# Performance work log

Hardware: AMD Instinct MI355X
Metric: run time of the kernel (lower is better)

## Reference

```python
import jax, jax.numpy as jnp
import numpy as np

B, S, D = 1, 2048, 4096
N_Q, N_KV, HD = 32, 8, 128
N_REP = N_Q // N_KV
WINDOW = 1024
NEG = -1e9


def setup_inputs() -> dict:
    key = jax.random.key(0)
    ks = jax.random.split(key, 6)
    x = jax.random.normal(ks[0], (B, S, D), dtype=jnp.float32)
    # RoPE frequencies (Llama-style): theta = 10000^{-2i/HD}
    inv_freq = 1.0 / (10000.0 ** (np.arange(0, HD, 2, dtype=np.float32) / HD))
    t = np.arange(S, dtype=np.float32)
    ang = np.outer(t, inv_freq)  # [S, HD//2]
    freqs_cos = jnp.asarray(np.cos(ang), dtype=jnp.float32)
    freqs_sin = jnp.asarray(np.sin(ang), dtype=jnp.float32)
    # additive causal mask [S, S]: 0 on/below diag, -1e9 above
    mask = jnp.where(jnp.tril(jnp.ones((S, S), dtype=bool)), 0.0, NEG).astype(jnp.float32)
    scale = 0.02
    w_q = jax.random.normal(ks[1], (D, N_Q * HD), dtype=jnp.float32) * scale
    w_k = jax.random.normal(ks[2], (D, N_KV * HD), dtype=jnp.float32) * scale
    w_v = jax.random.normal(ks[3], (D, N_KV * HD), dtype=jnp.float32) * scale
    w_o = jax.random.normal(ks[4], (N_Q * HD, D), dtype=jnp.float32) * scale
    return {"x": x, "freqs_cos": freqs_cos, "freqs_sin": freqs_sin, "mask": mask,
            "w_q": w_q, "w_k": w_k, "w_v": w_v, "w_o": w_o}


def _rope(t, cos, sin):
    # t: [B, S, H, HD]; cos/sin: [S, HD//2] -> complex multiply on pairs
    tp = t.reshape(*t.shape[:-1], HD // 2, 2)
    e, o = tp[..., 0], tp[..., 1]
    c = cos[None, :, None, :]
    s = sin[None, :, None, :]
    re = e * c - o * s
    ro = e * s + o * c
    return jnp.stack([re, ro], axis=-1).reshape(t.shape)


def reference(x, freqs_cos, freqs_sin, mask, w_q, w_k, w_v, w_o):
    b, s, _ = x.shape
    xq = (x @ w_q).reshape(b, s, N_Q, HD)
    xk = (x @ w_k).reshape(b, s, N_KV, HD)
    xv = (x @ w_v).reshape(b, s, N_KV, HD)
    xq = _rope(xq, freqs_cos, freqs_sin)
    xk = _rope(xk, freqs_cos, freqs_sin)
    # GQA head repeat
    keys = jnp.repeat(xk, N_REP, axis=2)    # [b, s, N_Q, HD]
    values = jnp.repeat(xv, N_REP, axis=2)
    q = xq.transpose(0, 2, 1, 3)            # [b, h, s, hd]
    k = keys.transpose(0, 2, 1, 3)
    v = values.transpose(0, 2, 1, 3)
    scores = jnp.einsum('bhqd,bhkd->bhqk', q, k) / jnp.sqrt(jnp.float32(HD))
    scores = scores + mask[None, None, :, :]
    # sliding-window band: attend only to keys within WINDOW positions back
    idx = jnp.arange(s)
    diff = idx[:, None] - idx[None, :]
    sliding = (diff >= 0) & (diff < WINDOW)
    scores = jnp.where(sliding[None, None, :, :], scores, NEG)
    probs = jax.nn.softmax(scores, axis=-1).astype(q.dtype)
    out = jnp.einsum('bhqk,bhkd->bhqd', probs, v)
    out = out.transpose(0, 2, 1, 3).reshape(b, s, N_Q * HD)
    return out @ w_o
```

## Files before the change

kernel.cpp:

```cpp
#include <hip/hip_runtime.h>

typedef unsigned short u16;
typedef unsigned int u32;
typedef __bf16 bf16x8 __attribute__((ext_vector_type(8)));
typedef __bf16 bf16x4 __attribute__((ext_vector_type(4)));
typedef float f32x4 __attribute__((ext_vector_type(4)));

#define MFMA16(a, b, c) __builtin_amdgcn_mfma_f32_16x16x32_bf16(a, b, c, 0, 0, 0)

__device__ __forceinline__ u16 f2bf(float f) {
  u32 u = __float_as_uint(f);
  u += 0x7FFFu + ((u >> 16) & 1u);
  return (u16)(u >> 16);
}
__device__ __forceinline__ float bf2f(u16 h) {
  return __uint_as_float(((u32)h) << 16);
}

__device__ __forceinline__ void gload_lds16(const u16* g, u16* l) {
  __builtin_amdgcn_global_load_lds((__attribute__((address_space(1))) void*)g,
                                   (__attribute__((address_space(3))) void*)l,
                                   16, 0, 0);
}

__global__ __launch_bounds__(256) void cvt_x(const float* __restrict__ in,
                                             u16* __restrict__ out) {
  int i = (blockIdx.x * 256 + threadIdx.x) * 4;
  float4 v = *(const float4*)&in[i];
  ushort4 o;
  o.x = f2bf(v.x);
  o.y = f2bf(v.y);
  o.z = f2bf(v.z);
  o.w = f2bf(v.w);
  *(ushort4*)&out[i] = o;
}

__global__ __launch_bounds__(256) void tbf_f2b(const float* __restrict__ in,
                                               u16* __restrict__ out,
                                               int ldin, int ldout) {
  __shared__ float tile[64][65];
  const int t = threadIdx.x;
  const int c4 = t & 15;
  const int rb = t >> 4;
  const int r0 = blockIdx.y * 64;
  const int c0 = blockIdx.x * 64;
#pragma unroll
  for (int p = 0; p < 4; p++) {
    int r = p * 16 + rb;
    float4 v = *(const float4*)&in[(size_t)(r0 + r) * ldin + c0 + c4 * 4];
    tile[r][c4 * 4 + 0] = v.x;
    tile[r][c4 * 4 + 1] = v.y;
    tile[r][c4 * 4 + 2] = v.z;
    tile[r][c4 * 4 + 3] = v.w;
  }
  __syncthreads();
#pragma unroll
  for (int p = 0; p < 4; p++) {
    int oc = p * 16 + rb;
    ushort4 v;
    v.x = f2bf(tile[c4 * 4 + 0][oc]);
    v.y = f2bf(tile[c4 * 4 + 1][oc]);
    v.z = f2bf(tile[c4 * 4 + 2][oc]);
    v.w = f2bf(tile[c4 * 4 + 3][oc]);
    *(ushort4*)&out[(size_t)(c0 + oc) * ldout + r0 + c4 * 4] = v;
  }
}

__global__ __launch_bounds__(256) void tbf_b(const u16* __restrict__ in,
                                             u16* __restrict__ out,
                                             int ldin, int ldout) {
  __shared__ u16 tile[64][68];
  const int t = threadIdx.x;
  const int c4 = t & 15;
  const int rb = t >> 4;
  const int r0 = blockIdx.y * 64;
  const int c0 = blockIdx.x * 64;
#pragma unroll
  for (int p = 0; p < 4; p++) {
    int r = p * 16 + rb;
    ushort4 v = *(const ushort4*)&in[(size_t)(r0 + r) * ldin + c0 + c4 * 4];
    *(ushort4*)&tile[r][c4 * 4] = v;
  }
  __syncthreads();
#pragma unroll
  for (int p = 0; p < 4; p++) {
    int oc = p * 16 + rb;
    ushort4 v;
    v.x = tile[c4 * 4 + 0][oc];
    v.y = tile[c4 * 4 + 1][oc];
    v.z = tile[c4 * 4 + 2][oc];
    v.w = tile[c4 * 4 + 3][oc];
    *(ushort4*)&out[(size_t)(c0 + oc) * ldout + r0 + c4 * 4] = v;
  }
}

template <int BM, int BN, int WM, int WN, int F32OUT>
__global__ __launch_bounds__(512, 2) void gemm3(const u16* __restrict__ A,
                                                const u16* __restrict__ B,
                                                void* __restrict__ Cv,
                                                int K, int ldc) {
  constexpr int R = BM / WM / 16;
  constexpr int C = BN / WN / 16;
  constexpr int LA = (BM * 4) / 512;
  constexpr int EXTRA = BN * 4 - 512;
  constexpr int MG = (2048 / BM) / 8;
  __shared__ __attribute__((aligned(16))) u16 As[3][BM * 32];
  __shared__ __attribute__((aligned(16))) u16 Bs[3][BN * 32];
  const int tid = threadIdx.x;
  const int wave = tid >> 6;
  const int lane = tid & 63;
  const int l16 = lane & 15;
  const int quad = lane >> 4;
  const int wm = wave / WN;
  const int wn = wave % WN;
  const int id = blockIdx.x;
  const int bm = ((id & 7) * MG + ((id >> 3) % MG)) * BM;
  const int bn0 = ((id >> 3) / MG) * BN;

  const u16* srcA[LA];
#pragma unroll
  for (int m = 0; m < LA; m++) {
    int c = m * 512 + tid;
    int r = c >> 2;
    int hl = (c & 3) ^ (r & 3) ^ ((r >> 2) & 3);
    srcA[m] = A + (size_t)(bm + r) * K + hl * 8;
  }
  const u16* srcB0;
  const u16* srcB1;
  {
    int c = tid, r = c >> 2;
    int hl = (c & 3) ^ (r & 3) ^ ((r >> 2) & 3);
    srcB0 = B + (size_t)(bn0 + r) * K + hl * 8;
    c = 512 + tid;
    r = c >> 2;
    int r2 = r < BN ? r : 0;
    hl = (c & 3) ^ (r2 & 3) ^ ((r2 >> 2) & 3);
    srcB1 = B + (size_t)(bn0 + r2) * K + hl * 8;
  }

  f32x4 acc[R][C];
#pragma unroll
  for (int i = 0; i < R; i++)
#pragma unroll
    for (int j = 0; j < C; j++) acc[i][j] = (f32x4){0.f, 0.f, 0.f, 0.f};

  auto stage = [&](int kt, int nb2) {
    const int ko = kt * 32;
#pragma unroll
    for (int m = 0; m < LA; m++)
      gload_lds16(srcA[m] + ko, &As[nb2][(m * 512 + tid) * 8]);
    gload_lds16(srcB0 + ko, &Bs[nb2][tid * 8]);
    if constexpr (EXTRA == 512) {
      gload_lds16(srcB1 + ko, &Bs[nb2][(512 + tid) * 8]);
    } else if constexpr (EXTRA > 0) {
      if (tid < EXTRA) gload_lds16(srcB1 + ko, &Bs[nb2][(512 + tid) * 8]);
    }
  };

  const int NT = K >> 5;
  stage(0, 0);
  stage(1, 1);
  int nb = 0, ns = 2;
  for (int t = 0; t < NT; ++t) {
    if (t == NT - 1) {
      asm volatile("s_waitcnt vmcnt(0)" ::: "memory");
    } else if constexpr (EXTRA == 512) {
      asm volatile("s_waitcnt vmcnt(3)" ::: "memory");
    } else {
      if (wave < 4)
        asm volatile("s_waitcnt vmcnt(4)" ::: "memory");
      else
        asm volatile("s_waitcnt vmcnt(3)" ::: "memory");
    }
    __builtin_amdgcn_sched_barrier(0);
    __builtin_amdgcn_s_barrier();
    __builtin_amdgcn_sched_barrier(0);
    if (t + 2 < NT) stage(t + 2, ns);

    const u16* as = &As[nb][0];
    const u16* bs = &Bs[nb][0];
    bf16x8 bfr[C];
#pragma unroll
    for (int j = 0; j < C; j++) {
      int r = wn * (C * 16) + j * 16 + l16;
      bfr[j] = *(const bf16x8*)&bs[r * 32 +
                                   ((quad ^ (r & 3) ^ ((r >> 2) & 3)) << 3)];
    }
    bf16x8 afr[R];
#pragma unroll
    for (int i = 0; i < R; i++) {
      int r = wm * (R * 16) + i * 16 + l16;
      afr[i] = *(const bf16x8*)&as[r * 32 +
                                   ((quad ^ (r & 3) ^ ((r >> 2) & 3)) << 3)];
    }
    __builtin_amdgcn_s_setprio(1);
#pragma unroll
    for (int i = 0; i < R; i++)
#pragma unroll
      for (int j = 0; j < C; j++)
        acc[i][j] = MFMA16(afr[i], bfr[j], acc[i][j]);
    __builtin_amdgcn_s_setprio(0);
    __builtin_amdgcn_sched_barrier(0);
    nb = (nb == 2) ? 0 : nb + 1;
    ns = (ns == 2) ? 0 : ns + 1;
  }

  const int crow0 = bm + wm * (R * 16);
  const int ccol0 = bn0 + wn * (C * 16);
  if constexpr (F32OUT) {
    float* Cp = (float*)Cv;
#pragma unroll
    for (int i = 0; i < R; i++)
#pragma unroll
      for (int j = 0; j < C; j++)
#pragma unroll
        for (int rr = 0; rr < 4; rr++) {
          int row = crow0 + i * 16 + quad * 4 + rr;
          int col = ccol0 + j * 16 + l16;
          Cp[(size_t)row * ldc + col] = acc[i][j][rr];
        }
  } else {
    u16* Cp = (u16*)Cv;
#pragma unroll
    for (int i = 0; i < R; i++)
#pragma unroll
      for (int j = 0; j < C; j++)
#pragma unroll
        for (int rr = 0; rr < 4; rr++) {
          int row = crow0 + i * 16 + quad * 4 + rr;
          int col = ccol0 + j * 16 + l16;
          Cp[(size_t)row * ldc + col] = f2bf(acc[i][j][rr]);
        }
  }
}

__global__ __launch_bounds__(256) void rope_k(u16* __restrict__ qkv,
                                              const float* __restrict__ fc,
                                              const float* __restrict__ fs) {
  int idx = blockIdx.x * 256 + threadIdx.x;
  int j = idx & 63;
  int rem = idx >> 6;
  int head = rem % 40;
  int s = rem / 40;
  float c = fc[s * 64 + j];
  float sn = fs[s * 64 + j];
  int col = (head < 32) ? (head * 128 + 2 * j) : (4096 + (head - 32) * 128 + 2 * j);
  u32* p = (u32*)&qkv[(size_t)s * 6144 + col];
  u32 v = *p;
  float e = bf2f((u16)(v & 0xFFFFu));
  float o = bf2f((u16)(v >> 16));
  float re = e * c - o * sn;
  float ro = e * sn + o * c;
  *p = (u32)f2bf(re) | ((u32)f2bf(ro) << 16);
}

__global__ __launch_bounds__(256) void attn_k(const u16* __restrict__ qkv,
                                              const u16* __restrict__ vt,
                                              u16* __restrict__ outb) {
  __shared__ __attribute__((aligned(16))) u16 Kb[2][32 * 128];
  __shared__ __attribute__((aligned(16))) u16 Vb[2][128 * 32];
  __shared__ __attribute__((aligned(16))) u16 plds[4][32 * 36];
  const int h = blockIdx.x;
  const int q0 = blockIdx.y * 128;
  const int t = threadIdx.x;
  const int wave = t >> 6;
  const int lane = t & 63;
  const int l16 = lane & 15;
  const int quad = lane >> 4;
  const int hkv = h >> 2;
  const int qw = q0 + wave * 32;
  u16* myp = &plds[wave][0];

  bf16x8 qa[2][4];
#pragma unroll
  for (int i = 0; i < 2; i++)
#pragma unroll
    for (int kc = 0; kc < 4; kc++)
      qa[i][kc] = *(const bf16x8*)&qkv[(size_t)(qw + i * 16 + l16) * 6144 +
                                       h * 128 + kc * 32 + quad * 8];

  f32x4 o[2][8];
#pragma unroll
  for (int i = 0; i < 2; i++)
#pragma unroll
    for (int d = 0; d < 8; d++) o[i][d] = (f32x4){0.f, 0.f, 0.f, 0.f};
  float lloc[2][4] = {{0.f, 0.f, 0.f, 0.f}, {0.f, 0.f, 0.f, 0.f}};

  const int kb_start = (q0 - 1023 > 0 ? q0 - 1023 : 0) & ~31;
  const int kb_last = q0 + 96;
  const float sc = 0.08838834764831845f;

  const int kr0 = t >> 4, kc0s = t & 15;
  const int kr1 = (256 + t) >> 4, kc1s = t & 15;
  const int vr0 = t >> 2, vc0s = t & 3;
  const int vr1 = (256 + t) >> 2, vc1s = t & 3;
  const u16* kg = qkv + 4096 + hkv * 128;
  const u16* vg = vt + (size_t)hkv * 128 * 2048;

#define STAGE(kb_, nb_)                                                        \
  do {                                                                         \
    int kb__ = (kb_);                                                          \
    gload_lds16(&kg[(size_t)(kb__ + kr0) * 6144 + (kc0s ^ (kr0 & 15)) * 8],    \
                &Kb[nb_][t * 8]);                                              \
    gload_lds16(&kg[(size_t)(kb__ + kr1) * 6144 + (kc1s ^ (kr1 & 15)) * 8],    \
                &Kb[nb_][2048 + t * 8]);                                       \
    gload_lds16(&vg[(size_t)vr0 * 2048 + kb__ + (vc0s ^ (vr0 & 3)) * 8],       \
                &Vb[nb_][t * 8]);                                              \
    gload_lds16(&vg[(size_t)vr1 * 2048 + kb__ + (vc1s ^ (vr1 & 3)) * 8],       \
                &Vb[nb_][2048 + t * 8]);                                       \
  } while (0)

  STAGE(kb_start, 0);
  int cur = 0;

  for (int kb = kb_start; kb <= kb_last; kb += 32) {
    __syncthreads();
    if (kb + 32 <= kb_last) STAGE(kb + 32, cur ^ 1);
    const u16* kcur = &Kb[cur][0];
    const u16* vcur = &Vb[cur][0];

    f32x4 s0[2] = {(f32x4){0.f, 0.f, 0.f, 0.f}, (f32x4){0.f, 0.f, 0.f, 0.f}};
    f32x4 s1[2] = {(f32x4){0.f, 0.f, 0.f, 0.f}, (f32x4){0.f, 0.f, 0.f, 0.f}};
#pragma unroll
    for (int kc = 0; kc < 4; kc++) {
      int ch = ((kc * 4 + quad) ^ l16) * 8;
      bf16x8 b0 = *(const bf16x8*)&kcur[l16 * 128 + ch];
      bf16x8 b1 = *(const bf16x8*)&kcur[(l16 + 16) * 128 + ch];
      s0[0] = MFMA16(qa[0][kc], b0, s0[0]);
      s1[0] = MFMA16(qa[0][kc], b1, s1[0]);
      s0[1] = MFMA16(qa[1][kc], b0, s0[1]);
      s1[1] = MFMA16(qa[1][kc], b1, s1[1]);
    }

    float p0[2][4], p1[2][4];
    bool fast = (kb + 31 <= qw) && (qw + 31 - kb <= 1023);
    if (fast) {
#pragma unroll
      for (int i = 0; i < 2; i++)
#pragma unroll
        for (int r = 0; r < 4; r++) {
          p0[i][r] = __expf(s0[i][r] * sc);
          p1[i][r] = __expf(s1[i][r] * sc);
        }
    } else {
#pragma unroll
      for (int i = 0; i < 2; i++)
#pragma unroll
        for (int r = 0; r < 4; r++) {
          int row = qw + i * 16 + quad * 4 + r;
          int col0 = kb + l16;
          int col1 = col0 + 16;
          bool v0 = (col0 <= row) && (row - col0 < 1024);
          bool v1 = (col1 <= row) && (row - col1 < 1024);
          p0[i][r] = v0 ? __expf(s0[i][r] * sc) : 0.f;
          p1[i][r] = v1 ? __expf(s1[i][r] * sc) : 0.f;
        }
    }
#pragma unroll
    for (int i = 0; i < 2; i++)
#pragma unroll
      for (int r = 0; r < 4; r++) {
        lloc[i][r] += p0[i][r] + p1[i][r];
        myp[(i * 16 + quad * 4 + r) * 36 + l16] = f2bf(p0[i][r]);
        myp[(i * 16 + quad * 4 + r) * 36 + l16 + 16] = f2bf(p1[i][r]);
      }
    asm volatile("s_waitcnt lgkmcnt(0)" ::: "memory");
    bf16x8 pa[2];
#pragma unroll
    for (int i = 0; i < 2; i++) {
      bf16x4 lo = *(const bf16x4*)&myp[(i * 16 + l16) * 36 + quad * 8];
      bf16x4 hi = *(const bf16x4*)&myp[(i * 16 + l16) * 36 + quad * 8 + 4];
#pragma unroll
      for (int j = 0; j < 4; j++) {
        pa[i][j] = lo[j];
        pa[i][j + 4] = hi[j];
      }
    }
#pragma unroll
    for (int d = 0; d < 8; d++) {
      int rv = l16 + 16 * d;
      bf16x8 vb = *(const bf16x8*)&vcur[rv * 32 + ((quad ^ (l16 & 3)) * 8)];
      o[0][d] = MFMA16(pa[0], vb, o[0][d]);
      o[1][d] = MFMA16(pa[1], vb, o[1][d]);
    }
    cur ^= 1;
  }

#pragma unroll
  for (int i = 0; i < 2; i++) {
    float inv[4];
#pragma unroll
    for (int r = 0; r < 4; r++) {
      float l = lloc[i][r];
#pragma unroll
      for (int m = 8; m >= 1; m >>= 1) l += __shfl_xor(l, m, 64);
      inv[r] = 1.0f / l;
    }
#pragma unroll
    for (int d = 0; d < 8; d++)
#pragma unroll
      for (int r = 0; r < 4; r++) {
        int row = qw + i * 16 + quad * 4 + r;
        outb[(size_t)row * 4096 + h * 128 + d * 16 + l16] =
            f2bf(o[i][d][r] * inv[r]);
      }
  }
#undef STAGE
}

extern "C" void kernel_launch(void* const* d_in, const int* in_sizes, int n_in,
                              void* d_out, int out_size, void* d_ws, size_t ws_size,
                              hipStream_t stream) {
  const float* x = (const float*)d_in[0];
  const float* fc = (const float*)d_in[1];
  const float* fs = (const float*)d_in[2];
  const float* wq = (const float*)d_in[4];
  const float* wk = (const float*)d_in[5];
  const float* wv = (const float*)d_in[6];
  const float* wo = (const float*)d_in[7];
  float* outp = (float*)d_out;
  char* ws = (char*)d_ws;
  u16* xb = (u16*)(ws);
  u16* wqkvT = (u16*)(ws + 16777216);
  u16* qkvb = (u16*)(ws + 67108864);
  u16* vtb = (u16*)(ws + 92274688);
  u16* aout = (u16*)(ws + 96468992);

  cvt_x<<<8192, 256, 0, stream>>>(x, xb);
  tbf_f2b<<<dim3(64, 64), 256, 0, stream>>>(wq, wqkvT, 4096, 4096);
  tbf_f2b<<<dim3(16, 64), 256, 0, stream>>>(wk, wqkvT + (size_t)4096 * 4096,
                                            1024, 4096);
  tbf_f2b<<<dim3(16, 64), 256, 0, stream>>>(wv, wqkvT + (size_t)5120 * 4096,
                                            1024, 4096);
  gemm3<256, 192, 4, 2, 0><<<256, 512, 0, stream>>>(xb, wqkvT, qkvb, 4096,
                                                    6144);
  rope_k<<<20480, 256, 0, stream>>>(qkvb, fc, fs);
  tbf_b<<<dim3(16, 32), 256, 0, stream>>>(qkvb + 5120, vtb, 6144, 2048);
  tbf_f2b<<<dim3(64, 64), 256, 0, stream>>>(wo, wqkvT, 4096, 4096);
  attn_k<<<dim3(32, 16), 256, 0, stream>>>(qkvb, vtb, aout);
  gemm3<128, 256, 2, 4, 1><<<256, 512, 0, stream>>>(aout, wqkvT, outp, 4096,
                                                    4096);
}
```

Baseline: 561.0 us.

## Rework GEMM into double-buffered 64-wide K tiles with split-phase MFMA and barriers

Replaces the triple-buffered 32-wide-K GEMM with a double-buffered kernel that stages 64-wide K tiles. It uses a new 8-way XOR swizzle, a fixed 256-row M tile with a 4x2 wave grid, and splits each K step into two sub-steps and two N-phases separated by barriers. The output GEMM changes from a 128x256 tile to 256x128. The aim is to halve the number of load/barrier iterations, interleave LDS reads with MFMA issue, and reduce bank conflicts. In exchange it adds extra intra-iteration barriers, uses more LDS per block, and drops the grouped block-index swizzle used for L2 locality.

```diff
diff --git a/kernel.cpp b/kernel.cpp
--- a/kernel.cpp
+++ b/kernel.cpp
@@ -94,48 +94,45 @@
   }
 }
 
-template <int BM, int BN, int WM, int WN, int F32OUT>
-__global__ __launch_bounds__(512, 2) void gemm3(const u16* __restrict__ A,
+template <int BN, int F32OUT>
+__global__ __launch_bounds__(512, 2) void gemmp(const u16* __restrict__ A,
                                                 const u16* __restrict__ B,
                                                 void* __restrict__ Cv,
                                                 int K, int ldc) {
-  constexpr int R = BM / WM / 16;
-  constexpr int C = BN / WN / 16;
-  constexpr int LA = (BM * 4) / 512;
-  constexpr int EXTRA = BN * 4 - 512;
-  constexpr int MG = (2048 / BM) / 8;
-  __shared__ __attribute__((aligned(16))) u16 As[3][BM * 32];
-  __shared__ __attribute__((aligned(16))) u16 Bs[3][BN * 32];
+  constexpr int BM = 256;
+  constexpr int R = 4;
+  constexpr int C = BN / 32;
+  constexpr int CH = C / 2;
+  constexpr int LA = BM / 64;
+  constexpr int LB = BN / 64;
+  __shared__ __attribute__((aligned(16))) u16 As[2][BM * 64];
+  __shared__ __attribute__((aligned(16))) u16 Bs[2][BN * 64];
   const int tid = threadIdx.x;
   const int wave = tid >> 6;
   const int lane = tid & 63;
   const int l16 = lane & 15;
   const int quad = lane >> 4;
-  const int wm = wave / WN;
-  const int wn = wave % WN;
+  const int wm = wave >> 1;
+  const int wn = wave & 1;
   const int id = blockIdx.x;
-  const int bm = ((id & 7) * MG + ((id >> 3) % MG)) * BM;
-  const int bn0 = ((id >> 3) / MG) * BN;
+  const int bm = (id & 7) * BM;
+  const int bn0 = (id >> 3) * BN;
 
   const u16* srcA[LA];
 #pragma unroll
   for (int m = 0; m < LA; m++) {
     int c = m * 512 + tid;
-    int r = c >> 2;
-    int hl = (c & 3) ^ (r & 3) ^ ((r >> 2) & 3);
+    int r = c >> 3;
+    int hl = (c & 7) ^ (r & 7);
     srcA[m] = A + (size_t)(bm + r) * K + hl * 8;
   }
-  const u16* srcB0;
-  const u16* srcB1;
-  {
-    int c = tid, r = c >> 2;
-    int hl = (c & 3) ^ (r & 3) ^ ((r >> 2) & 3);
-    srcB0 = B + (size_t)(bn0 + r) * K + hl * 8;
-    c = 512 + tid;
-    r = c >> 2;
-    int r2 = r < BN ? r : 0;
-    hl = (c & 3) ^ (r2 & 3) ^ ((r2 >> 2) & 3);
-    srcB1 = B + (size_t)(bn0 + r2) * K + hl * 8;
+  const u16* srcB[LB];
+#pragma unroll
+  for (int m = 0; m < LB; m++) {
+    int c = m * 512 + tid;
+    int r = c >> 3;
+    int hl = (c & 7) ^ (r & 7);
+    srcB[m] = B + (size_t)(bn0 + r) * K + hl * 8;
   }
 
   f32x4 acc[R][C];
@@ -144,68 +141,68 @@
 #pragma unroll
     for (int j = 0; j < C; j++) acc[i][j] = (f32x4){0.f, 0.f, 0.f, 0.f};
 
-  auto stage = [&](int kt, int nb2) {
-    const int ko = kt * 32;
+  auto stage = [&](int ko, int buf) {
 #pragma unroll
     for (int m = 0; m < LA; m++)
-      gload_lds16(srcA[m] + ko, &As[nb2][(m * 512 + tid) * 8]);
-    gload_lds16(srcB0 + ko, &Bs[nb2][tid * 8]);
-    if constexpr (EXTRA == 512) {
-      gload_lds16(srcB1 + ko, &Bs[nb2][(512 + tid) * 8]);
-    } else if constexpr (EXTRA > 0) {
-      if (tid < EXTRA) gload_lds16(srcB1 + ko, &Bs[nb2][(512 + tid) * 8]);
-    }
+      gload_lds16(srcA[m] + ko, &As[buf][(m * 512 + tid) * 8]);
+#pragma unroll
+    for (int m = 0; m < LB; m++)
+      gload_lds16(srcB[m] + ko, &Bs[buf][(m * 512 + tid) * 8]);
   };
 
-  const int NT = K >> 5;
+  const int NT = K >> 6;
   stage(0, 0);
-  stage(1, 1);
-  int nb = 0, ns = 2;
   for (int t = 0; t < NT; ++t) {
-    if (t == NT - 1) {
+    if (t + 1 < NT) {
+      stage((t + 1) << 6, (t + 1) & 1);
+      if constexpr (LA + LB == 7)
+        asm volatile("s_waitcnt vmcnt(7)" ::: "memory");
+      else
+        asm volatile("s_waitcnt vmcnt(6)" ::: "memory");
+    } else {
       asm volatile("s_waitcnt vmcnt(0)" ::: "memory");
-    } else if constexpr (EXTRA == 512) {
-      asm volatile("s_waitcnt vmcnt(3)" ::: "memory");
-    } else {
-      if (wave < 4)
-        asm volatile("s_waitcnt vmcnt(4)" ::: "memory");
-      else
-        asm volatile("s_waitcnt vmcnt(3)" ::: "memory");
     }
     __builtin_amdgcn_sched_barrier(0);
     __builtin_amdgcn_s_barrier();
     __builtin_amdgcn_sched_barrier(0);
-    if (t + 2 < NT) stage(t + 2, ns);
-
-    const u16* as = &As[nb][0];
-    const u16* bs = &Bs[nb][0];
-    bf16x8 bfr[C];
-#pragma unroll
-    for (int j = 0; j < C; j++) {
-      int r = wn * (C * 16) + j * 16 + l16;
-      bfr[j] = *(const bf16x8*)&bs[r * 32 +
-                                   ((quad ^ (r & 3) ^ ((r >> 2) & 3)) << 3)];
-    }
+
+    const u16* as = &As[t & 1][0];
+    const u16* bs = &Bs[t & 1][0];
     bf16x8 afr[R];
 #pragma unroll
-    for (int i = 0; i < R; i++) {
-      int r = wm * (R * 16) + i * 16 + l16;
-      afr[i] = *(const bf16x8*)&as[r * 32 +
-                                   ((quad ^ (r & 3) ^ ((r >> 2) & 3)) << 3)];
-    }
-    __builtin_amdgcn_s_setprio(1);
-#pragma unroll
-    for (int i = 0; i < R; i++)
-#pragma unroll
-      for (int j = 0; j < C; j++)
-        acc[i][j] = MFMA16(afr[i], bfr[j], acc[i][j]);
-    __builtin_amdgcn_s_setprio(0);
-    __builtin_amdgcn_sched_barrier(0);
-    nb = (nb == 2) ? 0 : nb + 1;
-    ns = (ns == 2) ? 0 : ns + 1;
-  }
-
-  const int crow0 = bm + wm * (R * 16);
+    for (int ks = 0; ks < 2; ks++) {
+#pragma unroll
+      for (int ph = 0; ph < 2; ph++) {
+        if (ph == 0) {
+#pragma unroll
+          for (int i = 0; i < R; i++) {
+            int row = wm * 64 + i * 16 + l16;
+            afr[i] = *(const bf16x8*)
+                &as[row * 64 + (((ks * 4 + quad) ^ (row & 7)) << 3)];
+          }
+        }
+        bf16x8 bfr[CH];
+#pragma unroll
+        for (int j = 0; j < CH; j++) {
+          int row = wn * (C * 16) + (ph * CH + j) * 16 + l16;
+          bfr[j] = *(const bf16x8*)
+              &bs[row * 64 + (((ks * 4 + quad) ^ (row & 7)) << 3)];
+        }
+        __builtin_amdgcn_s_setprio(1);
+#pragma unroll
+        for (int i = 0; i < R; i++)
+#pragma unroll
+          for (int j = 0; j < CH; j++)
+            acc[i][ph * CH + j] = MFMA16(afr[i], bfr[j], acc[i][ph * CH + j]);
+        __builtin_amdgcn_s_setprio(0);
+        __builtin_amdgcn_sched_barrier(0);
+        __builtin_amdgcn_s_barrier();
+        __builtin_amdgcn_sched_barrier(0);
+      }
+    }
+  }
+
+  const int crow0 = bm + wm * 64;
   const int ccol0 = bn0 + wn * (C * 16);
   if constexpr (F32OUT) {
     float* Cp = (float*)Cv;
@@ -432,12 +429,10 @@
                                             1024, 4096);
   tbf_f2b<<<dim3(16, 64), 256, 0, stream>>>(wv, wqkvT + (size_t)5120 * 4096,
                                             1024, 4096);
-  gemm3<256, 192, 4, 2, 0><<<256, 512, 0, stream>>>(xb, wqkvT, qkvb, 4096,
-                                                    6144);
+  gemmp<192, 0><<<256, 512, 0, stream>>>(xb, wqkvT, qkvb, 4096, 6144);
   rope_k<<<20480, 256, 0, stream>>>(qkvb, fc, fs);
   tbf_b<<<dim3(16, 32), 256, 0, stream>>>(qkvb + 5120, vtb, 6144, 2048);
   tbf_f2b<<<dim3(64, 64), 256, 0, stream>>>(wo, wqkvT, 4096, 4096);
   attn_k<<<dim3(32, 16), 256, 0, stream>>>(qkvb, vtb, aout);
-  gemm3<128, 256, 2, 4, 1><<<256, 512, 0, stream>>>(aout, wqkvT, outp, 4096,
-                                                    4096);
-}
+  gemmp<128, 1><<<256, 512, 0, stream>>>(aout, wqkvT, outp, 4096, 4096);
+}
```

Result: faster. 526.7 us (-6.1%).
